# Performance work log

Measured on AMD Instinct MI355X. Metric: run time of the kernel, lower is better.

## Reference

```python
import jax, jax.numpy as jnp
import numpy as np

B, L, D, V, T = 4, 512, 2048, 32000, 1024


def setup_inputs() -> dict:
    key = jax.random.key(0)
    k1, k2, k3 = jax.random.split(key, 3)
    encoder_outs = jax.random.normal(k1, (B, L, D), dtype=jnp.float32)
    embed_weight = jax.random.normal(k2, (V, D), dtype=jnp.float32) * 0.02
    input_ids = jax.random.randint(k3, (B, T), 0, V)
    # encoder (audio) tokens occupy the prefix of the LLM input sequence
    modality_mask = jnp.broadcast_to(jnp.arange(T) < L, (B, T))
    return {
        "encoder_outs": encoder_outs,
        "embed_weight": embed_weight,
        "input_ids": input_ids,
        "modality_mask": modality_mask,
    }


def reference(encoder_outs, embed_weight, input_ids, modality_mask):
    # chunked matmul in torch == one big contraction: (B,L,D) x (V,D) -> (B,L,V)
    sim = jnp.einsum("bld,vd->blv", encoder_outs, embed_weight)
    enc_norm = jnp.sqrt(jnp.sum(jnp.square(encoder_outs), axis=-1, keepdims=True))
    w_norm = jnp.sqrt(jnp.sum(jnp.square(embed_weight), axis=-1))  # (V,)
    cosine = sim / enc_norm / w_norm[None, None, :]
    quantize_index = jnp.argmax(cosine, axis=-1)  # (B, L)
    enc_quant = embed_weight[quantize_index]      # (B, L, D) gather lookup

    inputs_embeds = embed_weight[input_ids]       # (B, T, D)
    # pad encoder tokens to full sequence length, then blend via modality mask
    enc_pad = jnp.pad(enc_quant, ((0, 0), (0, T - L), (0, 0)))
    blended = jnp.where(modality_mask[:, :, None], enc_pad, inputs_embeds)
    return blended, quantize_index
```

## Files before the change

kernel.cpp:

```cpp
#include <hip/hip_runtime.h>
#include <math.h>

typedef __attribute__((ext_vector_type(8))) short short8v;
typedef __attribute__((ext_vector_type(4))) float f32x4;
typedef unsigned long long u64;
typedef unsigned short ushort_t;

constexpr int Bb = 4;
constexpr int Ll = 512;
constexpr int Dk = 2048;
constexpr int Vv = 32000;
constexpr int Tt = 1024;
constexpr int Mrows = Bb * Ll;

constexpr int BM = 128;
constexpr int BN = 128;
constexpr int BK = 32;
constexpr int NVB = Vv / BN;
constexpr int KCAND = 8;

constexpr size_t WS_NEEDED = 147914752ull;

__device__ __forceinline__ unsigned int fkey(float f) {
    unsigned int u = __float_as_uint(f);
    return (u & 0x80000000u) ? ~u : (u | 0x80000000u);
}
__device__ __forceinline__ void top2(u64& b1, u64& b2, u64 p) {
    if (p > b1) { b2 = b1; b1 = p; }
    else if (p > b2) { b2 = p; }
}
__device__ __forceinline__ u64 shfl64(u64 x, int m) {
    unsigned lo = __shfl_xor((unsigned)x, m, 64);
    unsigned hi = __shfl_xor((unsigned)(x >> 32), m, 64);
    return ((u64)hi << 32) | lo;
}
__device__ __forceinline__ ushort_t bftrunc(float x) {
    return (ushort_t)(__float_as_uint(x) >> 16);
}
__device__ __forceinline__ void gload_lds16(const void* g, void* l) {
    __builtin_amdgcn_global_load_lds(
        (const __attribute__((address_space(1))) unsigned int*)g,
        (__attribute__((address_space(3))) unsigned int*)l, 16, 0, 0);
}

__global__ __launch_bounds__(256) void convertA_kernel(const float* __restrict__ A,
                                                       ushort_t* __restrict__ Ab) {
    int i = blockIdx.x * blockDim.x + threadIdx.x;
    const float4* src = (const float4*)A;
    float4 x = src[i * 2], y = src[i * 2 + 1];
    ushort_t o[8] = {bftrunc(x.x), bftrunc(x.y), bftrunc(x.z), bftrunc(x.w),
                     bftrunc(y.x), bftrunc(y.y), bftrunc(y.z), bftrunc(y.w)};
    *(int4*)(Ab + (size_t)i * 8) = *(const int4*)o;
}

__global__ __launch_bounds__(256) void convertW_kernel(const float* __restrict__ W,
                                                       ushort_t* __restrict__ Wb,
                                                       float* __restrict__ winv) {
    int wave = (blockIdx.x * blockDim.x + threadIdx.x) >> 6;
    int lane = threadIdx.x & 63;
    if (wave >= Vv) return;
    const float4* row = (const float4*)(W + (size_t)wave * Dk);
    ushort4* orow = (ushort4*)(Wb + (size_t)wave * Dk);
    float s = 0.f;
#pragma unroll
    for (int i = 0; i < Dk / 4 / 64; ++i) {
        float4 v = row[lane + 64 * i];
        s = fmaf(v.x, v.x, s); s = fmaf(v.y, v.y, s);
        s = fmaf(v.z, v.z, s); s = fmaf(v.w, v.w, s);
        ushort4 o;
        o.x = bftrunc(v.x); o.y = bftrunc(v.y);
        o.z = bftrunc(v.z); o.w = bftrunc(v.w);
        orow[lane + 64 * i] = o;
    }
#pragma unroll
    for (int off = 32; off; off >>= 1) s += __shfl_down(s, off, 64);
    if (lane == 0) winv[wave] = 1.0f / sqrtf(s);
}

__global__ __launch_bounds__(256) void wnorm_kernel(const float* __restrict__ W,
                                                    float* __restrict__ winv) {
    int wave = (blockIdx.x * blockDim.x + threadIdx.x) >> 6;
    int lane = threadIdx.x & 63;
    if (wave >= Vv) return;
    const float4* row = (const float4*)(W + (size_t)wave * Dk);
    float s = 0.f;
#pragma unroll
    for (int i = 0; i < Dk / 4 / 64; ++i) {
        float4 v = row[lane + 64 * i];
        s = fmaf(v.x, v.x, s); s = fmaf(v.y, v.y, s);
        s = fmaf(v.z, v.z, s); s = fmaf(v.w, v.w, s);
    }
#pragma unroll
    for (int off = 32; off; off >>= 1) s += __shfl_down(s, off, 64);
    if (lane == 0) winv[wave] = 1.0f / sqrtf(s);
}

__global__ void init_best_kernel(u64* __restrict__ best) {
    int i = blockIdx.x * blockDim.x + threadIdx.x;
    if (i < Mrows) best[i] = 0ull;
}

template <typename LdsT>
__device__ __forceinline__ void topk_epilogue(f32x4 (&acc)[4][4], LdsT* ldsbase,
                                              const float* __restrict__ winv,
                                              u64* __restrict__ cand, int row0, int v0,
                                              int vby, int tid, int lane, int wr, int wc) {
    const int cbase = v0 + wc * 64 + (lane & 15);
    float wv[4];
#pragma unroll
    for (int nf = 0; nf < 4; ++nf) wv[nf] = winv[cbase + nf * 16];

    u64(*red)[4] = (u64(*)[4])ldsbase;
#pragma unroll
    for (int mf = 0; mf < 4; ++mf) {
#pragma unroll
        for (int reg = 0; reg < 4; ++reg) {
            u64 b1 = 0, b2 = 0;
#pragma unroll
            for (int nf = 0; nf < 4; ++nf) {
                float s = acc[mf][nf][reg] * wv[nf];
                int v = cbase + nf * 16;
                u64 p = ((u64)fkey(s) << 32) | (unsigned)(Vv - 1 - v);
                top2(b1, b2, p);
            }
#pragma unroll
            for (int m = 1; m < 16; m <<= 1) {
                u64 o1 = shfl64(b1, m);
                u64 o2 = shfl64(b2, m);
                top2(b1, b2, o1);
                top2(b1, b2, o2);
            }
            if ((lane & 15) == 0) {
                int rl = wr * 64 + mf * 16 + ((lane >> 4) << 2) + reg;
                red[rl][wc * 2] = b1;
                red[rl][wc * 2 + 1] = b2;
            }
        }
    }
    __syncthreads();
    if (tid < BM) {
        u64 b1 = red[tid][0], b2 = red[tid][1];
        top2(b1, b2, red[tid][2]);
        top2(b1, b2, red[tid][3]);
        u64* c = cand + (size_t)(row0 + tid) * (2 * NVB) + vby * 2;
        c[0] = b1;
        c[1] = b2;
    }
}

__global__ __launch_bounds__(256) void score_topk_kernel(
    const ushort_t* __restrict__ Ab, const ushort_t* __restrict__ Wb,
    const float* __restrict__ winv, u64* __restrict__ cand) {
    __shared__ __align__(16) ushort_t Alds[4096];
    __shared__ __align__(16) ushort_t Wlds[4096];

    const int tid = threadIdx.x;
    const int row0 = blockIdx.x * BM;
    const int v0 = blockIdx.y * BN;
    const int lane = tid & 63;
    const int wid = tid >> 6;
    const int wr = wid >> 1, wc = wid & 1;

    const int s0 = wid * 2, s1 = wid * 2 + 1;
    const int rsub = lane & 15;
    const int ksub = (lane >> 4) * 8;

    const ushort_t* pa0 = Ab + (size_t)(row0 + s0 * 16 + rsub) * Dk + ksub;
    const ushort_t* pa1 = Ab + (size_t)(row0 + s1 * 16 + rsub) * Dk + ksub;
    const ushort_t* pw0 = Wb + (size_t)(v0 + s0 * 16 + rsub) * Dk + ksub;
    const ushort_t* pw1 = Wb + (size_t)(v0 + s1 * 16 + rsub) * Dk + ksub;

    ushort_t* la0 = &Alds[s0 * 512];
    ushort_t* la1 = &Alds[s1 * 512];
    ushort_t* lw0 = &Wlds[s0 * 512];
    ushort_t* lw1 = &Wlds[s1 * 512];

    f32x4 acc[4][4];
#pragma unroll
    for (int i = 0; i < 4; ++i)
#pragma unroll
        for (int j = 0; j < 4; ++j) acc[i][j] = (f32x4){0.f, 0.f, 0.f, 0.f};

    for (int kt = 0; kt < Dk / BK; ++kt) {
        const int ko = kt * BK;
        gload_lds16(pa0 + ko, la0);
        gload_lds16(pa1 + ko, la1);
        gload_lds16(pw0 + ko, lw0);
        gload_lds16(pw1 + ko, lw1);
        __syncthreads();
        short8v af[4], bf[4];
        const short8v* Ap = (const short8v*)Alds;
        const short8v* Wp = (const short8v*)Wlds;
#pragma unroll
        for (int mf = 0; mf < 4; ++mf) af[mf] = Ap[(wr * 4 + mf) * 64 + lane];
#pragma unroll
        for (int nf = 0; nf < 4; ++nf) bf[nf] = Wp[(wc * 4 + nf) * 64 + lane];
#pragma unroll
        for (int mf = 0; mf < 4; ++mf)
#pragma unroll
            for (int nf = 0; nf < 4; ++nf)
                acc[mf][nf] = __builtin_amdgcn_mfma_f32_16x16x32_bf16(
                    af[mf], bf[nf], acc[mf][nf], 0, 0, 0);
        __syncthreads();
    }

    topk_epilogue(acc, Alds, winv, cand, row0, v0, blockIdx.y, tid, lane, wr, wc);
}

__global__ __launch_bounds__(256) void score_topk_fallback(
    const float* __restrict__ A, const float* __restrict__ W,
    const float* __restrict__ winv, u64* __restrict__ cand) {
    __shared__ __align__(16) short Albuf[4096];
    __shared__ __align__(16) short Wlbuf[4096];

    const int tid = threadIdx.x;
    const int row0 = blockIdx.x * BM;
    const int v0 = blockIdx.y * BN;
    const int lane = tid & 63;
    const int wid = tid >> 6;
    const int wr = wid >> 1, wc = wid & 1;

    const int rA = ((tid >> 6) << 4) + (tid & 15);
    const int kk = ((tid >> 4) & 3) * 8;

    const float* pa = A + (size_t)(row0 + rA) * Dk + kk;
    const float* pw = W + (size_t)(v0 + rA) * Dk + kk;

    float4 fa0, fa1, fa2, fa3, fw0, fw1, fw2, fw3;
    auto ld4 = [](const float* p) { return *(const float4*)p; };
    auto load_regs = [&](int k0) {
        fa0 = ld4(pa + k0); fa1 = ld4(pa + k0 + 4);
        fa2 = ld4(pa + k0 + (size_t)64 * Dk); fa3 = ld4(pa + k0 + (size_t)64 * Dk + 4);
        fw0 = ld4(pw + k0); fw1 = ld4(pw + k0 + 4);
        fw2 = ld4(pw + k0 + (size_t)64 * Dk); fw3 = ld4(pw + k0 + (size_t)64 * Dk + 4);
    };
    auto pk = [](float lo, float hi) {
        return (int)((__float_as_uint(lo) >> 16) | (__float_as_uint(hi) & 0xFFFF0000u));
    };
    auto cv = [&](float4 a, float4 b) {
        int4 r; r.x = pk(a.x, a.y); r.y = pk(a.z, a.w);
        r.z = pk(b.x, b.y); r.w = pk(b.z, b.w); return r;
    };
    auto write_lds = [&]() {
        *(int4*)(Albuf + tid * 8) = cv(fa0, fa1);
        *(int4*)(Albuf + tid * 8 + 2048) = cv(fa2, fa3);
        *(int4*)(Wlbuf + tid * 8) = cv(fw0, fw1);
        *(int4*)(Wlbuf + tid * 8 + 2048) = cv(fw2, fw3);
    };

    f32x4 acc[4][4];
#pragma unroll
    for (int i = 0; i < 4; ++i)
#pragma unroll
        for (int j = 0; j < 4; ++j) acc[i][j] = (f32x4){0.f, 0.f, 0.f, 0.f};

    load_regs(0);
    for (int kt = 0; kt < Dk / BK; ++kt) {
        write_lds();
        __syncthreads();
        if (kt + 1 < Dk / BK) load_regs((kt + 1) * BK);
        short8v af[4], bf[4];
        const short8v* Ap = (const short8v*)Albuf;
        const short8v* Wp = (const short8v*)Wlbuf;
#pragma unroll
        for (int mf = 0; mf < 4; ++mf) af[mf] = Ap[(wr * 4 + mf) * 64 + lane];
#pragma unroll
        for (int nf = 0; nf < 4; ++nf) bf[nf] = Wp[(wc * 4 + nf) * 64 + lane];
#pragma unroll
        for (int mf = 0; mf < 4; ++mf)
#pragma unroll
            for (int nf = 0; nf < 4; ++nf)
                acc[mf][nf] = __builtin_amdgcn_mfma_f32_16x16x32_bf16(
                    af[mf], bf[nf], acc[mf][nf], 0, 0, 0);
        __syncthreads();
    }

    topk_epilogue(acc, Albuf, winv, cand, row0, v0, blockIdx.y, tid, lane, wr, wc);
}

__global__ __launch_bounds__(256) void topk_kernel(const u64* __restrict__ cand,
                                                   int* __restrict__ sel) {
    int row = blockIdx.x * 4 + (threadIdx.x >> 6);
    int lane = threadIdx.x & 63;
    if (row >= Mrows) return;
    const u64* c = cand + (size_t)row * (2 * NVB);
    u64 v[8];
#pragma unroll
    for (int i = 0; i < 8; ++i) {
        int idx = lane + i * 64;
        v[i] = (idx < 2 * NVB) ? c[idx] : 0ull;
    }
#pragma unroll
    for (int it = 0; it < KCAND; ++it) {
        u64 lm = 0;
#pragma unroll
        for (int i = 0; i < 8; ++i) lm = v[i] > lm ? v[i] : lm;
#pragma unroll
        for (int m = 32; m; m >>= 1) {
            u64 o = shfl64(lm, m);
            lm = o > lm ? o : lm;
        }
#pragma unroll
        for (int i = 0; i < 8; ++i)
            if (v[i] == lm) v[i] = 0;
        if (lane == 0) sel[row * KCAND + it] = Vv - 1 - (int)(unsigned)(lm & 0xFFFFFFFFu);
    }
}

__global__ __launch_bounds__(256) void rescore_kernel(
    const float* __restrict__ A, const float* __restrict__ W,
    const float* __restrict__ winv, const int* __restrict__ sel,
    u64* __restrict__ best) {
    int gw = (int)((blockIdx.x * blockDim.x + threadIdx.x) >> 6);
    int lane = threadIdx.x & 63;
    if (gw >= Mrows * KCAND) return;
    int row = gw >> 3, c = gw & 7;
    int v = sel[row * KCAND + c];
    const float4* a = (const float4*)(A + (size_t)row * Dk);
    const float4* w = (const float4*)(W + (size_t)v * Dk);
    float s = 0.f;
#pragma unroll
    for (int i = 0; i < Dk / 4 / 64; ++i) {
        float4 x = a[lane + 64 * i], y = w[lane + 64 * i];
        s = fmaf(x.x, y.x, s); s = fmaf(x.y, y.y, s);
        s = fmaf(x.z, y.z, s); s = fmaf(x.w, y.w, s);
    }
#pragma unroll
    for (int m = 32; m; m >>= 1) s += __shfl_xor(s, m, 64);
    if (lane == 0) {
        u64 p = ((u64)fkey(s * winv[v]) << 32) | (unsigned)(Vv - 1 - v);
        atomicMax(best + row, p);
    }
}

__global__ __launch_bounds__(256) void blend_kernel(
    const float* __restrict__ emb, const int* __restrict__ ids,
    const u64* __restrict__ best, float* __restrict__ out) {
    int row = blockIdx.x;
    int b = row / Tt;
    int t = row % Tt;
    int idx;
    if (t < Ll) {
        idx = Vv - 1 - (int)(best[b * Ll + t] & 0xFFFFFFFFu);
    } else {
        idx = ids[row];
    }
    const float4* src = (const float4*)(emb + (size_t)idx * Dk);
    float4* dst = (float4*)(out + (size_t)row * Dk);
    for (int i = threadIdx.x; i < Dk / 4; i += blockDim.x) dst[i] = src[i];
    if (t < Ll && threadIdx.x == 0) {
        out[(size_t)Bb * Tt * Dk + (size_t)(b * Ll + t)] = (float)idx;
    }
}

extern "C" void kernel_launch(void* const* d_in, const int* in_sizes, int n_in,
                              void* d_out, int out_size, void* d_ws, size_t ws_size,
                              hipStream_t stream) {
    const float* encoder_outs = (const float*)d_in[0];
    const float* embed_weight = (const float*)d_in[1];
    const int* input_ids = (const int*)d_in[2];

    float* out = (float*)d_out;

    float* winv = (float*)d_ws;
    u64* best = (u64*)((char*)d_ws + 131072);
    int* sel = (int*)((char*)d_ws + 147456);
    u64* cand = (u64*)((char*)d_ws + 262144);
    ushort_t* Abf = (ushort_t*)((char*)d_ws + 8454144);
    ushort_t* Wbf = (ushort_t*)((char*)d_ws + 16842752);

    dim3 grid(Mrows / BM, Vv / BN);
    init_best_kernel<<<(Mrows + 255) / 256, 256, 0, stream>>>(best);

    if (ws_size >= WS_NEEDED) {
        convertA_kernel<<<Mrows * Dk / 8 / 256, 256, 0, stream>>>(encoder_outs, Abf);
        convertW_kernel<<<Vv * 64 / 256, 256, 0, stream>>>(embed_weight, Wbf, winv);
        score_topk_kernel<<<grid, 256, 0, stream>>>(Abf, Wbf, winv, cand);
    } else {
        wnorm_kernel<<<Vv * 64 / 256, 256, 0, stream>>>(embed_weight, winv);
        score_topk_fallback<<<grid, 256, 0, stream>>>(encoder_outs, embed_weight, winv,
                                                      cand);
    }
    topk_kernel<<<Mrows / 4, 256, 0, stream>>>(cand, sel);
    rescore_kernel<<<Mrows * KCAND / 4, 256, 0, stream>>>(encoder_outs, embed_weight,
                                                          winv, sel, best);
    blend_kernel<<<Bb * Tt, 256, 0, stream>>>(embed_weight, input_ids, best, out);
}
```

Before: 1.172 ms.

## Triple-buffer LDS loads in score kernel and swizzle blocks across XCDs

After: 1.171 ms. No clear change (-0.0%).

```diff
diff --git a/kernel.cpp b/kernel.cpp
--- a/kernel.cpp
+++ b/kernel.cpp
@@ -18,6 +18,10 @@
 constexpr int BK = 32;
 constexpr int NVB = Vv / BN;
 constexpr int KCAND = 8;
+constexpr int NT = Dk / BK;
+constexpr int NWGX = Mrows / BM;
+constexpr int NWG = NWGX * NVB;
+constexpr int CHUNK = NWG / 8;
 
 constexpr size_t WS_NEEDED = 147914752ull;
 
@@ -151,12 +155,17 @@
 __global__ __launch_bounds__(256) void score_topk_kernel(
     const ushort_t* __restrict__ Ab, const ushort_t* __restrict__ Wb,
     const float* __restrict__ winv, u64* __restrict__ cand) {
-    __shared__ __align__(16) ushort_t Alds[4096];
-    __shared__ __align__(16) ushort_t Wlds[4096];
+    __shared__ __align__(16) ushort_t Alds[3][4096];
+    __shared__ __align__(16) ushort_t Wlds[3][4096];
+
+    const int orig = blockIdx.x;
+    const int swz = (orig & 7) * CHUNK + (orig >> 3);
+    const int bx = swz & (NWGX - 1);
+    const int by = swz >> 4;
+    const int row0 = bx * BM;
+    const int v0 = by * BN;
 
     const int tid = threadIdx.x;
-    const int row0 = blockIdx.x * BM;
-    const int v0 = blockIdx.y * BN;
     const int lane = tid & 63;
     const int wid = tid >> 6;
     const int wr = wid >> 1, wc = wid & 1;
@@ -170,10 +179,13 @@
     const ushort_t* pw0 = Wb + (size_t)(v0 + s0 * 16 + rsub) * Dk + ksub;
     const ushort_t* pw1 = Wb + (size_t)(v0 + s1 * 16 + rsub) * Dk + ksub;
 
-    ushort_t* la0 = &Alds[s0 * 512];
-    ushort_t* la1 = &Alds[s1 * 512];
-    ushort_t* lw0 = &Wlds[s0 * 512];
-    ushort_t* lw1 = &Wlds[s1 * 512];
+    auto stage = [&](int buf, int kt) {
+        const int ko = kt * BK;
+        gload_lds16(pa0 + ko, &Alds[buf][s0 * 512]);
+        gload_lds16(pa1 + ko, &Alds[buf][s1 * 512]);
+        gload_lds16(pw0 + ko, &Wlds[buf][s0 * 512]);
+        gload_lds16(pw1 + ko, &Wlds[buf][s1 * 512]);
+    };
 
     f32x4 acc[4][4];
 #pragma unroll
@@ -181,16 +193,10 @@
 #pragma unroll
         for (int j = 0; j < 4; ++j) acc[i][j] = (f32x4){0.f, 0.f, 0.f, 0.f};
 
-    for (int kt = 0; kt < Dk / BK; ++kt) {
-        const int ko = kt * BK;
-        gload_lds16(pa0 + ko, la0);
-        gload_lds16(pa1 + ko, la1);
-        gload_lds16(pw0 + ko, lw0);
-        gload_lds16(pw1 + ko, lw1);
-        __syncthreads();
+    auto compute_tile = [&](int buf) {
         short8v af[4], bf[4];
-        const short8v* Ap = (const short8v*)Alds;
-        const short8v* Wp = (const short8v*)Wlds;
+        const short8v* Ap = (const short8v*)&Alds[buf][0];
+        const short8v* Wp = (const short8v*)&Wlds[buf][0];
 #pragma unroll
         for (int mf = 0; mf < 4; ++mf) af[mf] = Ap[(wr * 4 + mf) * 64 + lane];
 #pragma unroll
@@ -201,10 +207,34 @@
             for (int nf = 0; nf < 4; ++nf)
                 acc[mf][nf] = __builtin_amdgcn_mfma_f32_16x16x32_bf16(
                     af[mf], bf[nf], acc[mf][nf], 0, 0, 0);
-        __syncthreads();
-    }
-
-    topk_epilogue(acc, Alds, winv, cand, row0, v0, blockIdx.y, tid, lane, wr, wc);
+    };
+
+    stage(0, 0);
+    stage(1, 1);
+    stage(2, 2);
+
+    int buf = 0;
+    for (int kt = 0; kt < NT; ++kt) {
+        if (kt <= NT - 3)
+            asm volatile("s_waitcnt vmcnt(8)" ::: "memory");
+        else if (kt == NT - 2)
+            asm volatile("s_waitcnt vmcnt(4)" ::: "memory");
+        else
+            asm volatile("s_waitcnt vmcnt(0)" ::: "memory");
+        __builtin_amdgcn_s_barrier();
+        asm volatile("" ::: "memory");
+
+        compute_tile(buf);
+
+        asm volatile("" ::: "memory");
+        __builtin_amdgcn_s_barrier();
+        asm volatile("" ::: "memory");
+        if (kt + 3 < NT) stage(buf, kt + 3);
+
+        buf = (buf == 2) ? 0 : buf + 1;
+    }
+
+    topk_epilogue(acc, &Alds[0][0], winv, cand, row0, v0, by, tid, lane, wr, wc);
 }
 
 __global__ __launch_bounds__(256) void score_topk_fallback(
@@ -369,15 +399,15 @@
     ushort_t* Abf = (ushort_t*)((char*)d_ws + 8454144);
     ushort_t* Wbf = (ushort_t*)((char*)d_ws + 16842752);
 
-    dim3 grid(Mrows / BM, Vv / BN);
     init_best_kernel<<<(Mrows + 255) / 256, 256, 0, stream>>>(best);
 
     if (ws_size >= WS_NEEDED) {
         convertA_kernel<<<Mrows * Dk / 8 / 256, 256, 0, stream>>>(encoder_outs, Abf);
         convertW_kernel<<<Vv * 64 / 256, 256, 0, stream>>>(embed_weight, Wbf, winv);
-        score_topk_kernel<<<grid, 256, 0, stream>>>(Abf, Wbf, winv, cand);
+        score_topk_kernel<<<NWG, 256, 0, stream>>>(Abf, Wbf, winv, cand);
     } else {
         wnorm_kernel<<<Vv * 64 / 256, 256, 0, stream>>>(embed_weight, winv);
+        dim3 grid(Mrows / BM, Vv / BN);
         score_topk_fallback<<<grid, 256, 0, stream>>>(encoder_outs, embed_weight, winv,
                                                       cand);
     }
```

## Enlarge score GEMM tiles to 256x256 with double-buffered LDS and grid swizzle

Applied to the files above, without the earlier changes.

New measurement: 1.116 ms. 4.8% less time.

```diff
diff --git a/kernel.cpp b/kernel.cpp
--- a/kernel.cpp
+++ b/kernel.cpp
@@ -13,11 +13,21 @@
 constexpr int Tt = 1024;
 constexpr int Mrows = Bb * Ll;
 
-constexpr int BM = 128;
-constexpr int BN = 128;
-constexpr int BK = 32;
-constexpr int NVB = Vv / BN;
+constexpr int BM = 256;
+constexpr int BN = 256;
+constexpr int BK = 64;
+constexpr int NKT = Dk / BK;
+constexpr int NBX = Mrows / BM;
+constexpr int NBY = Vv / BN;
+constexpr int NWG = NBX * NBY;
+constexpr int CHUNK = NWG / 8;
+
 constexpr int KCAND = 8;
+constexpr int CAND_STRIDE = 500;
+
+constexpr int FBM = 128;
+constexpr int FBN = 128;
+constexpr int FNVB = Vv / FBN;
 
 constexpr size_t WS_NEEDED = 147914752ull;
 
@@ -100,11 +110,131 @@
     if (i < Mrows) best[i] = 0ull;
 }
 
+__global__ __launch_bounds__(512, 2) void score_topk_kernel(
+    const ushort_t* __restrict__ Ab, const ushort_t* __restrict__ Wb,
+    const float* __restrict__ winv, u64* __restrict__ cand) {
+    __shared__ __align__(16) ushort_t Alds[2][16384];
+    __shared__ __align__(16) ushort_t Wlds[2][16384];
+
+    const int orig = blockIdx.x;
+    const int swz = (orig & 7) * CHUNK + (orig >> 3);
+    const int bx = swz & (NBX - 1);
+    const int by = swz >> 3;
+    const int row0 = bx * BM;
+    const int v0 = by * BN;
+
+    const int tid = threadIdx.x;
+    const int lane = tid & 63;
+    const int w = tid >> 6;
+    const int wr = w >> 2;
+    const int wc = w & 3;
+
+    const int rsub = lane & 15;
+    const int ksub = (lane >> 4) * 8;
+
+    const ushort_t* srcA[4];
+    const ushort_t* srcW[4];
+#pragma unroll
+    for (int q = 0; q < 4; ++q) {
+        const int fb = w * 4 + q, sub = fb >> 1, kk = fb & 1;
+        srcA[q] = Ab + (size_t)(row0 + sub * 16 + rsub) * Dk + kk * 32 + ksub;
+        srcW[q] = Wb + (size_t)(v0 + sub * 16 + rsub) * Dk + kk * 32 + ksub;
+    }
+
+    auto stage = [&](int buf, int t) {
+        const int k0 = t * BK;
+#pragma unroll
+        for (int q = 0; q < 4; ++q) {
+            const int fb = w * 4 + q;
+            gload_lds16(srcA[q] + k0, &Alds[buf][fb * 512]);
+            gload_lds16(srcW[q] + k0, &Wlds[buf][fb * 512]);
+        }
+    };
+
+    f32x4 acc[8][4];
+#pragma unroll
+    for (int i = 0; i < 8; ++i)
+#pragma unroll
+        for (int j = 0; j < 4; ++j) acc[i][j] = (f32x4){0.f, 0.f, 0.f, 0.f};
+
+    stage(0, 0);
+    __syncthreads();
+    int cur = 0;
+    for (int t = 0; t < NKT; ++t) {
+        if (t + 1 < NKT) stage(cur ^ 1, t + 1);
+        const short8v* Ap = (const short8v*)&Alds[cur][0];
+        const short8v* Wp = (const short8v*)&Wlds[cur][0];
+#pragma unroll
+        for (int kk = 0; kk < 2; ++kk) {
+            short8v a[8], b[4];
+#pragma unroll
+            for (int mf = 0; mf < 8; ++mf)
+                a[mf] = Ap[((wr * 8 + mf) * 2 + kk) * 64 + lane];
+#pragma unroll
+            for (int nf = 0; nf < 4; ++nf)
+                b[nf] = Wp[((wc * 4 + nf) * 2 + kk) * 64 + lane];
+            __builtin_amdgcn_s_setprio(1);
+#pragma unroll
+            for (int mf = 0; mf < 8; ++mf)
+#pragma unroll
+                for (int nf = 0; nf < 4; ++nf)
+                    acc[mf][nf] = __builtin_amdgcn_mfma_f32_16x16x32_bf16(
+                        a[mf], b[nf], acc[mf][nf], 0, 0, 0);
+            __builtin_amdgcn_s_setprio(0);
+        }
+        __syncthreads();
+        cur ^= 1;
+    }
+
+    const int cb = lane & 15;
+    float wv[4];
+#pragma unroll
+    for (int nf = 0; nf < 4; ++nf) wv[nf] = winv[v0 + wc * 64 + nf * 16 + cb];
+
+    u64(*red)[8] = (u64(*)[8]) & Alds[0][0];
+#pragma unroll
+    for (int mf = 0; mf < 8; ++mf) {
+#pragma unroll
+        for (int reg = 0; reg < 4; ++reg) {
+            u64 b1 = 0, b2 = 0;
+#pragma unroll
+            for (int nf = 0; nf < 4; ++nf) {
+                float s = acc[mf][nf][reg] * wv[nf];
+                int v = v0 + wc * 64 + nf * 16 + cb;
+                u64 p = ((u64)fkey(s) << 32) | (unsigned)(Vv - 1 - v);
+                top2(b1, b2, p);
+            }
+#pragma unroll
+            for (int m = 1; m < 16; m <<= 1) {
+                u64 o1 = shfl64(b1, m);
+                u64 o2 = shfl64(b2, m);
+                top2(b1, b2, o1);
+                top2(b1, b2, o2);
+            }
+            if (cb == 0) {
+                int rl = wr * 128 + mf * 16 + ((lane >> 4) << 2) + reg;
+                red[rl][wc * 2] = b1;
+                red[rl][wc * 2 + 1] = b2;
+            }
+        }
+    }
+    __syncthreads();
+    if (tid < BM) {
+        u64 b1 = red[tid][0], b2 = red[tid][1];
+#pragma unroll
+        for (int j = 2; j < 8; ++j) top2(b1, b2, red[tid][j]);
+        u64* c = cand + (size_t)(row0 + tid) * CAND_STRIDE + by * 2;
+        c[0] = b1;
+        c[1] = b2;
+    }
+}
+
 template <typename LdsT>
-__device__ __forceinline__ void topk_epilogue(f32x4 (&acc)[4][4], LdsT* ldsbase,
-                                              const float* __restrict__ winv,
-                                              u64* __restrict__ cand, int row0, int v0,
-                                              int vby, int tid, int lane, int wr, int wc) {
+__device__ __forceinline__ void topk_epilogue_f(f32x4 (&acc)[4][4], LdsT* ldsbase,
+                                                const float* __restrict__ winv,
+                                                u64* __restrict__ cand, int row0, int v0,
+                                                int vby, int tid, int lane, int wr,
+                                                int wc) {
     const int cbase = v0 + wc * 64 + (lane & 15);
     float wv[4];
 #pragma unroll
@@ -138,73 +268,14 @@
         }
     }
     __syncthreads();
-    if (tid < BM) {
+    if (tid < FBM) {
         u64 b1 = red[tid][0], b2 = red[tid][1];
         top2(b1, b2, red[tid][2]);
         top2(b1, b2, red[tid][3]);
-        u64* c = cand + (size_t)(row0 + tid) * (2 * NVB) + vby * 2;
+        u64* c = cand + (size_t)(row0 + tid) * CAND_STRIDE + vby * 2;
         c[0] = b1;
         c[1] = b2;
     }
-}
-
-__global__ __launch_bounds__(256) void score_topk_kernel(
-    const ushort_t* __restrict__ Ab, const ushort_t* __restrict__ Wb,
-    const float* __restrict__ winv, u64* __restrict__ cand) {
-    __shared__ __align__(16) ushort_t Alds[4096];
-    __shared__ __align__(16) ushort_t Wlds[4096];
-
-    const int tid = threadIdx.x;
-    const int row0 = blockIdx.x * BM;
-    const int v0 = blockIdx.y * BN;
-    const int lane = tid & 63;
-    const int wid = tid >> 6;
-    const int wr = wid >> 1, wc = wid & 1;
-
-    const int s0 = wid * 2, s1 = wid * 2 + 1;
-    const int rsub = lane & 15;
-    const int ksub = (lane >> 4) * 8;
-
-    const ushort_t* pa0 = Ab + (size_t)(row0 + s0 * 16 + rsub) * Dk + ksub;
-    const ushort_t* pa1 = Ab + (size_t)(row0 + s1 * 16 + rsub) * Dk + ksub;
-    const ushort_t* pw0 = Wb + (size_t)(v0 + s0 * 16 + rsub) * Dk + ksub;
-    const ushort_t* pw1 = Wb + (size_t)(v0 + s1 * 16 + rsub) * Dk + ksub;
-
-    ushort_t* la0 = &Alds[s0 * 512];
-    ushort_t* la1 = &Alds[s1 * 512];
-    ushort_t* lw0 = &Wlds[s0 * 512];
-    ushort_t* lw1 = &Wlds[s1 * 512];
-
-    f32x4 acc[4][4];
-#pragma unroll
-    for (int i = 0; i < 4; ++i)
-#pragma unroll
-        for (int j = 0; j < 4; ++j) acc[i][j] = (f32x4){0.f, 0.f, 0.f, 0.f};
-
-    for (int kt = 0; kt < Dk / BK; ++kt) {
-        const int ko = kt * BK;
-        gload_lds16(pa0 + ko, la0);
-        gload_lds16(pa1 + ko, la1);
-        gload_lds16(pw0 + ko, lw0);
-        gload_lds16(pw1 + ko, lw1);
-        __syncthreads();
-        short8v af[4], bf[4];
-        const short8v* Ap = (const short8v*)Alds;
-        const short8v* Wp = (const short8v*)Wlds;
-#pragma unroll
-        for (int mf = 0; mf < 4; ++mf) af[mf] = Ap[(wr * 4 + mf) * 64 + lane];
-#pragma unroll
-        for (int nf = 0; nf < 4; ++nf) bf[nf] = Wp[(wc * 4 + nf) * 64 + lane];
-#pragma unroll
-        for (int mf = 0; mf < 4; ++mf)
-#pragma unroll
-            for (int nf = 0; nf < 4; ++nf)
-                acc[mf][nf] = __builtin_amdgcn_mfma_f32_16x16x32_bf16(
-                    af[mf], bf[nf], acc[mf][nf], 0, 0, 0);
-        __syncthreads();
-    }
-
-    topk_epilogue(acc, Alds, winv, cand, row0, v0, blockIdx.y, tid, lane, wr, wc);
 }
 
 __global__ __launch_bounds__(256) void score_topk_fallback(
@@ -214,8 +285,8 @@
     __shared__ __align__(16) short Wlbuf[4096];
 
     const int tid = threadIdx.x;
-    const int row0 = blockIdx.x * BM;
-    const int v0 = blockIdx.y * BN;
+    const int row0 = blockIdx.x * FBM;
+    const int v0 = blockIdx.y * FBN;
     const int lane = tid & 63;
     const int wid = tid >> 6;
     const int wr = wid >> 1, wc = wid & 1;
@@ -255,10 +326,10 @@
         for (int j = 0; j < 4; ++j) acc[i][j] = (f32x4){0.f, 0.f, 0.f, 0.f};
 
     load_regs(0);
-    for (int kt = 0; kt < Dk / BK; ++kt) {
+    for (int kt = 0; kt < Dk / 32; ++kt) {
         write_lds();
         __syncthreads();
-        if (kt + 1 < Dk / BK) load_regs((kt + 1) * BK);
+        if (kt + 1 < Dk / 32) load_regs((kt + 1) * 32);
         short8v af[4], bf[4];
         const short8v* Ap = (const short8v*)Albuf;
         const short8v* Wp = (const short8v*)Wlbuf;
@@ -275,20 +346,20 @@
         __syncthreads();
     }
 
-    topk_epilogue(acc, Albuf, winv, cand, row0, v0, blockIdx.y, tid, lane, wr, wc);
+    topk_epilogue_f(acc, Albuf, winv, cand, row0, v0, blockIdx.y, tid, lane, wr, wc);
 }
 
 __global__ __launch_bounds__(256) void topk_kernel(const u64* __restrict__ cand,
-                                                   int* __restrict__ sel) {
+                                                   int* __restrict__ sel, int nents) {
     int row = blockIdx.x * 4 + (threadIdx.x >> 6);
     int lane = threadIdx.x & 63;
     if (row >= Mrows) return;
-    const u64* c = cand + (size_t)row * (2 * NVB);
+    const u64* c = cand + (size_t)row * CAND_STRIDE;
     u64 v[8];
 #pragma unroll
     for (int i = 0; i < 8; ++i) {
         int idx = lane + i * 64;
-        v[i] = (idx < 2 * NVB) ? c[idx] : 0ull;
+        v[i] = (idx < nents) ? c[idx] : 0ull;
     }
 #pragma unroll
     for (int it = 0; it < KCAND; ++it) {
@@ -369,19 +440,20 @@
     ushort_t* Abf = (ushort_t*)((char*)d_ws + 8454144);
     ushort_t* Wbf = (ushort_t*)((char*)d_ws + 16842752);
 
-    dim3 grid(Mrows / BM, Vv / BN);
     init_best_kernel<<<(Mrows + 255) / 256, 256, 0, stream>>>(best);
 
     if (ws_size >= WS_NEEDED) {
         convertA_kernel<<<Mrows * Dk / 8 / 256, 256, 0, stream>>>(encoder_outs, Abf);
         convertW_kernel<<<Vv * 64 / 256, 256, 0, stream>>>(embed_weight, Wbf, winv);
-        score_topk_kernel<<<grid, 256, 0, stream>>>(Abf, Wbf, winv, cand);
+        score_topk_kernel<<<NWG, 512, 0, stream>>>(Abf, Wbf, winv, cand);
+        topk_kernel<<<Mrows / 4, 256, 0, stream>>>(cand, sel, 2 * NBY);
     } else {
         wnorm_kernel<<<Vv * 64 / 256, 256, 0, stream>>>(embed_weight, winv);
+        dim3 grid(Mrows / FBM, Vv / FBN);
         score_topk_fallback<<<grid, 256, 0, stream>>>(encoder_outs, embed_weight, winv,
                                                       cand);
-    }
-    topk_kernel<<<Mrows / 4, 256, 0, stream>>>(cand, sel);
+        topk_kernel<<<Mrows / 4, 256, 0, stream>>>(cand, sel, 2 * FNVB);
+    }
     rescore_kernel<<<Mrows * KCAND / 4, 256, 0, stream>>>(encoder_outs, embed_weight,
                                                           winv, sel, best);
     blend_kernel<<<Bb * Tt, 256, 0, stream>>>(embed_weight, input_ids, best, out);
```
